# Kernel tuning notes

Hardware: AMD Instinct MI355X
Metric: run time of the kernel (lower is better)

The kernel has to match this reference:

```python
import jax, jax.numpy as jnp
import numpy as np

IN_FEATURES = 4096
IN_CHANNELS = 21
WINDOW = 32
STRIDES = 1
OUT_CHANNELS = 8
EPS = 1e-7
N_WIN = int((IN_FEATURES - WINDOW) / STRIDES - EPS) + 1  # 4064
NK = OUT_CHANNELS * N_WIN                                # 32512
D = IN_CHANNELS * WINDOW                                 # 672


def _window_starts():
    # windows 0..n_win-2 start at j*strides; last window anchored at in_features-window_size
    s = np.arange(N_WIN) * STRIDES
    s[-1] = IN_FEATURES - WINDOW
    return jnp.asarray(s, dtype=jnp.int32)


def setup_inputs() -> dict:
    key = jax.random.key(0)
    k1, k2 = jax.random.split(key)
    x = jax.random.normal(k1, (32, IN_CHANNELS, IN_FEATURES), dtype=jnp.float32)
    # matches torch init: 2*(rand-0.5)/sqrt(window_size*in_channels)
    weight = (jax.random.uniform(k2, (NK, D), dtype=jnp.float32) - 0.5) * 2.0 / np.sqrt(D)
    return {"x": x, "weight": weight}


def reference(x, weight):
    # x: (B, C, F); the sparse fbank matmul is an im2col gather of strided windows
    B = x.shape[0]
    starts = _window_starts()                        # (n_win,)
    idx = starts[:, None] + jnp.arange(WINDOW)       # (n_win, W)
    win = x[:, :, idx]                               # (B, C, n_win, W)
    # fbank row layout is channel-major (k, w) -> flatten as C*W
    win = jnp.transpose(win, (0, 2, 1, 3)).reshape(B, N_WIN, D)  # (B, n_win, C*W)
    # each window is replicated out_channels times in Nk; weight rows grouped per window
    w = weight.reshape(N_WIN, OUT_CHANNELS, D)
    out = jnp.einsum('bjd,jod->bjo', win, w)         # (B, n_win, out_channels)
    return out.reshape(B, NK)
```

## Files before the change

kernel.cpp:

```cpp
#include <hip/hip_runtime.h>
#include <hip/hip_bf16.h>


#define NF 4096
#define NC 21
#define WIN 32
#define OC 8
#define NWIN 4064
#define NKTOT (OC * NWIN)
#define DD (NC * WIN)
#define JB 8
#define NBLK (NWIN / JB)
#define XROWB 272
#define XBUFB 9216

typedef short short8 __attribute__((ext_vector_type(8)));
typedef float f32x4 __attribute__((ext_vector_type(4)));

static __device__ __forceinline__ short f2bf(float f) {
  __bf16 h = (__bf16)f;
  return __builtin_bit_cast(short, h);
}
static __device__ __forceinline__ short8 pk8(float a, float b, float c, float d,
                                             float e, float f, float g, float h) {
  short8 v;
  v[0]=f2bf(a); v[1]=f2bf(b); v[2]=f2bf(c); v[3]=f2bf(d);
  v[4]=f2bf(e); v[5]=f2bf(f); v[6]=f2bf(g); v[7]=f2bf(h);
  return v;
}
static __device__ __forceinline__ short8 sel8(f32x4 a, f32x4 b, f32x4 c, int u) {
  switch (u & 3) {
    case 0:  return pk8(a[0],a[1],a[2],a[3],b[0],b[1],b[2],b[3]);
    case 1:  return pk8(a[1],a[2],a[3],b[0],b[1],b[2],b[3],c[0]);
    case 2:  return pk8(a[2],a[3],b[0],b[1],b[2],b[3],c[0],c[1]);
    default: return pk8(a[3],b[0],b[1],b[2],b[3],c[0],c[1],c[2]);
  }
}

static __device__ __forceinline__ void wait_vmcnt(int n) {
  switch (n) {
    case 2: asm volatile("s_waitcnt vmcnt(2)" ::: "memory"); break;
    case 3: asm volatile("s_waitcnt vmcnt(3)" ::: "memory"); break;
    default: asm volatile("s_waitcnt vmcnt(4)" ::: "memory"); break;
  }
}

#define STAGE(GP, I, NB) \
  __builtin_amdgcn_global_load_lds( \
    (const __attribute__((address_space(1))) unsigned int*)(GP), \
    (__attribute__((address_space(3))) unsigned int*)(xlds + (NB)*XBUFB + (I)*1024), \
    16, 0, 0)

__global__ __launch_bounds__(512) void fb_pipe8(const float* __restrict__ x,
                                                const float* __restrict__ w,
                                                float* __restrict__ out) {
  __shared__ __align__(16) char xlds[3 * XBUFB];
  const int lane = threadIdx.x & 63;
  const int wv   = threadIdx.x >> 6;

  const int orig = blockIdx.x;
  const int xcd = orig & 7, idx = orig >> 3;
  const int blk = (xcd < 4 ? xcd * 64 : 256 + (xcd - 4) * 63) + idx;
  const int j0 = blk * JB;
  const int a0 = (j0 < NF - 68) ? j0 : (NF - 68);

  const int n  = lane & 15;
  const int o  = n & 7;
  const int Ck = (lane >> 4) * 2;
  const int boff0 = n * XROWB, boff1 = (16 + n) * XROWB;

  const int jg = j0 + wv;
  const int sv = (jg == NWIN - 1) ? (NF - WIN) : jg;
  const int rj = sv - a0;
  const int u  = rj & 3;
  const int Cw = rj >> 2;

  int q0 = wv * 64 + lane;
  int q2 = 512 + lane;
  if (q2 > 543) q2 = 543;
  const int b0 = q0 / 17, p0 = q0 - b0 * 17;
  const int b2 = q2 / 17, p2 = q2 - b2 * 17;
  const float* xs0 = x + (size_t)b0 * (NC * NF) + a0 + p0 * 4;
  const float* xs2 = x + (size_t)b2 * (NC * NF) + a0 + p2 * 4;

  const float* wn = w + ((size_t)jg * OC + o) * DD + Ck * 4;

  f32x4 acc0 = {0,0,0,0}, acc1 = {0,0,0,0};

  STAGE(xs0, wv, 0);
  if (wv == 0) { STAGE(xs2, 8, 0); }
  xs0 += NF; xs2 += NF;
  STAGE(xs0, wv, 1);
  if (wv == 0) { STAGE(xs2, 8, 1); }
  xs0 += NF; xs2 += NF;
  float4 wa = *(const float4*)(wn), wb = *(const float4*)(wn + 4);
  wn += WIN;

  const int STN = (wv == 0) ? 2 : 1;

  #pragma unroll
  for (int c = 0; c < NC; ++c) {
    if (c < NC - 1) wait_vmcnt(STN + 2);
    else            wait_vmcnt(2);
    __builtin_amdgcn_s_barrier();
    __builtin_amdgcn_sched_barrier(0);

    if (c + 2 < NC) {
      const int nb = (c + 2) % 3;
      STAGE(xs0, wv, nb);
      if (wv == 0) { STAGE(xs2, 8, nb); }
      xs0 += NF; xs2 += NF;
    }
    float4 wan = {0,0,0,0}, wbn = {0,0,0,0};
    if (c + 1 < NC) {
      wan = *(const float4*)(wn); wbn = *(const float4*)(wn + 4);
      wn += WIN;
    }

    const char* xb = xlds + (c % 3) * XBUFB;
    short8 fbw = pk8(wa.x, wa.y, wa.z, wa.w, wb.x, wb.y, wb.z, wb.w);
    {
      int off = boff0 + (Cw + Ck) * 16;
      f32x4 ra = *(const f32x4*)(xb + off);
      f32x4 rb = *(const f32x4*)(xb + off + 16);
      f32x4 rc = *(const f32x4*)(xb + off + 32);
      acc0 = __builtin_amdgcn_mfma_f32_16x16x32_bf16(sel8(ra,rb,rc,u), fbw, acc0, 0,0,0);
    }
    {
      int off = boff1 + (Cw + Ck) * 16;
      f32x4 ra = *(const f32x4*)(xb + off);
      f32x4 rb = *(const f32x4*)(xb + off + 16);
      f32x4 rc = *(const f32x4*)(xb + off + 32);
      acc1 = __builtin_amdgcn_mfma_f32_16x16x32_bf16(sel8(ra,rb,rc,u), fbw, acc1, 0,0,0);
    }
    wa = wan; wb = wbn;
  }

  if (n < 8) {
    const int m0 = (lane >> 4) * 4;
    #pragma unroll
    for (int e = 0; e < 4; ++e) {
      out[(size_t)(m0 + e)      * NKTOT + (size_t)jg * OC + n] = acc0[e];
      out[(size_t)(m0 + e + 16) * NKTOT + (size_t)jg * OC + n] = acc1[e];
    }
  }
}

extern "C" void kernel_launch(void* const* d_in, const int* in_sizes, int n_in,
                              void* d_out, int out_size, void* d_ws, size_t ws_size,
                              hipStream_t stream) {
  const float* x = (const float*)d_in[0];
  const float* w = (const float*)d_in[1];
  float* out = (float*)d_out;
  dim3 grid(NBLK), block(512);
  hipLaunchKernelGGL(fb_pipe8, grid, block, 0, stream, x, w, out);
}
```

Baseline: 30.05 us.

## Stage four channels per barrier with double-buffered LDS groups

```diff
diff --git a/kernel.cpp b/kernel.cpp
--- a/kernel.cpp
+++ b/kernel.cpp
@@ -13,6 +13,7 @@
 #define NBLK (NWIN / JB)
 #define XROWB 272
 #define XBUFB 9216
+#define GBUF (4 * XBUFB)
 
 typedef short short8 __attribute__((ext_vector_type(8)));
 typedef float f32x4 __attribute__((ext_vector_type(4)));
@@ -20,6 +21,12 @@
 static __device__ __forceinline__ short f2bf(float f) {
   __bf16 h = (__bf16)f;
   return __builtin_bit_cast(short, h);
+}
+static __device__ __forceinline__ short8 pk8w(float4 a, float4 b) {
+  short8 v;
+  v[0]=f2bf(a.x); v[1]=f2bf(a.y); v[2]=f2bf(a.z); v[3]=f2bf(a.w);
+  v[4]=f2bf(b.x); v[5]=f2bf(b.y); v[6]=f2bf(b.z); v[7]=f2bf(b.w);
+  return v;
 }
 static __device__ __forceinline__ short8 pk8(float a, float b, float c, float d,
                                              float e, float f, float g, float h) {
@@ -37,107 +44,130 @@
   }
 }
 
-static __device__ __forceinline__ void wait_vmcnt(int n) {
-  switch (n) {
-    case 2: asm volatile("s_waitcnt vmcnt(2)" ::: "memory"); break;
-    case 3: asm volatile("s_waitcnt vmcnt(3)" ::: "memory"); break;
-    default: asm volatile("s_waitcnt vmcnt(4)" ::: "memory"); break;
-  }
-}
-
-#define STAGE(GP, I, NB) \
-  __builtin_amdgcn_global_load_lds( \
-    (const __attribute__((address_space(1))) unsigned int*)(GP), \
-    (__attribute__((address_space(3))) unsigned int*)(xlds + (NB)*XBUFB + (I)*1024), \
-    16, 0, 0)
-
-__global__ __launch_bounds__(512) void fb_pipe8(const float* __restrict__ x,
+__global__ __launch_bounds__(512, 4) void fb_v7(const float* __restrict__ x,
                                                 const float* __restrict__ w,
                                                 float* __restrict__ out) {
-  __shared__ __align__(16) char xlds[3 * XBUFB];
+  __shared__ __align__(16) char xlds[2 * GBUF];
   const int lane = threadIdx.x & 63;
   const int wv   = threadIdx.x >> 6;
 
   const int orig = blockIdx.x;
-  const int xcd = orig & 7, idx = orig >> 3;
-  const int blk = (xcd < 4 ? xcd * 64 : 256 + (xcd - 4) * 63) + idx;
+  const int xcd = orig & 7, sidx = orig >> 3;
+  const int blk = (xcd < 4 ? xcd * 64 : 256 + (xcd - 4) * 63) + sidx;
   const int j0 = blk * JB;
   const int a0 = (j0 < NF - 68) ? j0 : (NF - 68);
 
   const int n  = lane & 15;
   const int o  = n & 7;
-  const int Ck = (lane >> 4) * 2;
-  const int boff0 = n * XROWB, boff1 = (16 + n) * XROWB;
+  const int kq = lane >> 4;
 
   const int jg = j0 + wv;
   const int sv = (jg == NWIN - 1) ? (NF - WIN) : jg;
   const int rj = sv - a0;
   const int u  = rj & 3;
   const int Cw = rj >> 2;
+  const int off0 = n * XROWB + (Cw + 2 * kq) * 16;
+  const int off1 = (16 + n) * XROWB + (Cw + 2 * kq) * 16;
 
-  int q0 = wv * 64 + lane;
-  int q2 = 512 + lane;
-  if (q2 > 543) q2 = 543;
-  const int b0 = q0 / 17, p0 = q0 - b0 * 17;
-  const int b2 = q2 / 17, p2 = q2 - b2 * 17;
-  const float* xs0 = x + (size_t)b0 * (NC * NF) + a0 + p0 * 4;
-  const float* xs2 = x + (size_t)b2 * (NC * NF) + a0 + p2 * 4;
+  int xo[5], lo[5];
+  #pragma unroll
+  for (int k = 0; k < 5; ++k) {
+    const int q = wv + 8 * k;
+    const int cg = q / 9, ck = q - cg * 9;
+    int id = ck * 64 + lane; if (id > 543) id = 543;
+    const int bb = id / 17, pp = id - bb * 17;
+    xo[k] = (bb * NC + cg) * NF + a0 + pp * 4;
+    lo[k] = cg * XBUFB + bb * XROWB + pp * 16;
+  }
+  const int id5 = wv * 64 + lane;
+  const int b5 = id5 / 17, p5 = id5 - b5 * 17;
+  const int xo5 = (b5 * NC + 20) * NF + a0 + p5 * 4;
+  const int lo5 = b5 * XROWB + p5 * 16;
+  int id5b = 512 + lane; if (id5b > 543) id5b = 543;
+  const int b5b = id5b / 17, p5b = id5b - b5b * 17;
+  const int xo5b = (b5b * NC + 20) * NF + a0 + p5b * 4;
+  const int lo5b = b5b * XROWB + p5b * 16;
 
-  const float* wn = w + ((size_t)jg * OC + o) * DD + Ck * 4;
+  const float* wp = w + ((size_t)jg * OC + o) * DD + kq * 8;
 
   f32x4 acc0 = {0,0,0,0}, acc1 = {0,0,0,0};
 
-  STAGE(xs0, wv, 0);
-  if (wv == 0) { STAGE(xs2, 8, 0); }
-  xs0 += NF; xs2 += NF;
-  STAGE(xs0, wv, 1);
-  if (wv == 0) { STAGE(xs2, 8, 1); }
-  xs0 += NF; xs2 += NF;
-  float4 wa = *(const float4*)(wn), wb = *(const float4*)(wn + 4);
-  wn += WIN;
+#define GLL(GOFF, LOFF) \
+  __builtin_amdgcn_global_load_lds( \
+    (const __attribute__((address_space(1))) unsigned int*)(x + (GOFF)), \
+    (__attribute__((address_space(3))) unsigned int*)(xlds + (LOFF)), 16, 0, 0)
 
-  const int STN = (wv == 0) ? 2 : 1;
+#define STAGE_G(GG) { \
+    const int cb_ = ((GG) & 1) * GBUF, gb_ = (GG) * 4 * NF; \
+    GLL(xo[0] + gb_, cb_ + lo[0]); \
+    GLL(xo[1] + gb_, cb_ + lo[1]); \
+    GLL(xo[2] + gb_, cb_ + lo[2]); \
+    GLL(xo[3] + gb_, cb_ + lo[3]); \
+    if (wv < 4) GLL(xo[4] + gb_, cb_ + lo[4]); }
 
-  #pragma unroll
-  for (int c = 0; c < NC; ++c) {
-    if (c < NC - 1) wait_vmcnt(STN + 2);
-    else            wait_vmcnt(2);
-    __builtin_amdgcn_s_barrier();
-    __builtin_amdgcn_sched_barrier(0);
+#define STAGE_TAIL() { \
+    GLL(xo5, GBUF + lo5); \
+    if (wv == 0) GLL(xo5b, GBUF + lo5b); }
 
-    if (c + 2 < NC) {
-      const int nb = (c + 2) % 3;
-      STAGE(xs0, wv, nb);
-      if (wv == 0) { STAGE(xs2, 8, nb); }
-      xs0 += NF; xs2 += NF;
-    }
-    float4 wan = {0,0,0,0}, wbn = {0,0,0,0};
-    if (c + 1 < NC) {
-      wan = *(const float4*)(wn); wbn = *(const float4*)(wn + 4);
-      wn += WIN;
-    }
+#define LOADW(G, P) { \
+    const float* p_ = wp + (size_t)(G) * 4 * WIN; \
+    P##0a = *(const float4*)(p_);      P##0b = *(const float4*)(p_ + 4); \
+    P##1a = *(const float4*)(p_ + 32); P##1b = *(const float4*)(p_ + 36); \
+    P##2a = *(const float4*)(p_ + 64); P##2b = *(const float4*)(p_ + 68); \
+    P##3a = *(const float4*)(p_ + 96); P##3b = *(const float4*)(p_ + 100); }
 
-    const char* xb = xlds + (c % 3) * XBUFB;
-    short8 fbw = pk8(wa.x, wa.y, wa.z, wa.w, wb.x, wb.y, wb.z, wb.w);
-    {
-      int off = boff0 + (Cw + Ck) * 16;
-      f32x4 ra = *(const f32x4*)(xb + off);
-      f32x4 rb = *(const f32x4*)(xb + off + 16);
-      f32x4 rc = *(const f32x4*)(xb + off + 32);
-      acc0 = __builtin_amdgcn_mfma_f32_16x16x32_bf16(sel8(ra,rb,rc,u), fbw, acc0, 0,0,0);
-    }
-    {
-      int off = boff1 + (Cw + Ck) * 16;
-      f32x4 ra = *(const f32x4*)(xb + off);
-      f32x4 rb = *(const f32x4*)(xb + off + 16);
-      f32x4 rc = *(const f32x4*)(xb + off + 32);
-      acc1 = __builtin_amdgcn_mfma_f32_16x16x32_bf16(sel8(ra,rb,rc,u), fbw, acc1, 0,0,0);
-    }
-    wa = wan; wb = wbn;
-  }
+#define COMPUTE_CH(XB, WA, WB) { \
+    short8 fbw_ = pk8w(WA, WB); \
+    f32x4 ra_ = *(const f32x4*)((XB) + off0); \
+    f32x4 rb_ = *(const f32x4*)((XB) + off0 + 16); \
+    f32x4 rc_ = *(const f32x4*)((XB) + off0 + 32); \
+    acc0 = __builtin_amdgcn_mfma_f32_16x16x32_bf16(sel8(ra_,rb_,rc_,u), fbw_, acc0, 0,0,0); \
+    ra_ = *(const f32x4*)((XB) + off1); \
+    rb_ = *(const f32x4*)((XB) + off1 + 16); \
+    rc_ = *(const f32x4*)((XB) + off1 + 32); \
+    acc1 = __builtin_amdgcn_mfma_f32_16x16x32_bf16(sel8(ra_,rb_,rc_,u), fbw_, acc1, 0,0,0); }
+
+  float4 c0a, c0b, c1a, c1b, c2a, c2b, c3a, c3b;
+  float4 n0a, n0b, n1a, n1b, n2a, n2b, n3a, n3b;
+
+  STAGE_G(0);
+  LOADW(0, c);
+
+#define BODY4(G) { \
+    asm volatile("s_waitcnt vmcnt(8)" ::: "memory"); \
+    __builtin_amdgcn_s_barrier(); \
+    __builtin_amdgcn_sched_barrier(0); \
+    if ((G) < 4) { STAGE_G((G) + 1); LOADW((G) + 1, n); } \
+    else { \
+      STAGE_TAIL(); \
+      const float* p_ = wp + 20 * WIN; \
+      n0a = *(const float4*)(p_); n0b = *(const float4*)(p_ + 4); \
+    } \
+    __builtin_amdgcn_sched_barrier(0); \
+    const char* xb_ = xlds + ((G) & 1) * GBUF; \
+    COMPUTE_CH(xb_,             c0a, c0b); \
+    COMPUTE_CH(xb_ + XBUFB,     c1a, c1b); \
+    COMPUTE_CH(xb_ + 2*XBUFB,   c2a, c2b); \
+    COMPUTE_CH(xb_ + 3*XBUFB,   c3a, c3b); \
+    c0a = n0a; c0b = n0b; c1a = n1a; c1b = n1b; \
+    c2a = n2a; c2b = n2b; c3a = n3a; c3b = n3b; }
+
+  BODY4(0); BODY4(1); BODY4(2); BODY4(3); BODY4(4);
+
+  asm volatile("s_waitcnt vmcnt(2)" ::: "memory");
+  __builtin_amdgcn_s_barrier();
+  __builtin_amdgcn_sched_barrier(0);
+  COMPUTE_CH(xlds + GBUF, c0a, c0b);
+
+#undef BODY4
+#undef COMPUTE_CH
+#undef LOADW
+#undef STAGE_TAIL
+#undef STAGE_G
+#undef GLL
 
   if (n < 8) {
-    const int m0 = (lane >> 4) * 4;
+    const int m0 = kq * 4;
     #pragma unroll
     for (int e = 0; e < 4; ++e) {
       out[(size_t)(m0 + e)      * NKTOT + (size_t)jg * OC + n] = acc0[e];
@@ -153,5 +183,5 @@
   const float* w = (const float*)d_in[1];
   float* out = (float*)d_out;
   dim3 grid(NBLK), block(512);
-  hipLaunchKernelGGL(fb_pipe8, grid, block, 0, stream, x, w, out);
+  hipLaunchKernelGGL(fb_v7, grid, block, 0, stream, x, w, out);
 }
```

Measured after the change: 33.13 us. +10.3%, slower.
